# Performance work log

Measured on AMD Instinct MI355X. Metric: run time of the kernel, lower is better.

Reference implementation:

```python
import jax, jax.numpy as jnp
import numpy as np

N, E, IN, H, C, ED = 50000, 400000, 128, 16, 32, 16
NEG_SLOPE = 0.2

def setup_inputs() -> dict:
    key = jax.random.key(0)
    ks = jax.random.split(key, 9)
    x = jax.random.normal(ks[0], (N, IN), jnp.float32)
    edge_index = jax.random.randint(ks[1], (2, E), 0, N, dtype=jnp.int32)
    edge_attr = jax.random.normal(ks[2], (E, ED), jnp.float32)
    batch = jnp.zeros((N,), jnp.int32)
    W_l = jax.random.normal(ks[3], (IN, H * C), jnp.float32) * 0.05
    W_r = jax.random.normal(ks[4], (IN, H * C), jnp.float32) * 0.05
    att = jax.random.normal(ks[5], (H, C), jnp.float32) * 0.05
    bias_gat = jax.random.normal(ks[6], (C,), jnp.float32) * 0.05
    W_res = jax.random.normal(ks[7], (IN, C), jnp.float32) * 0.05
    return {"x": x, "edge_index": edge_index, "edge_attr": edge_attr, "batch": batch,
            "W_l": W_l, "W_r": W_r, "att": att, "bias_gat": bias_gat, "W_res": W_res}

def reference(x, edge_index, edge_attr, batch, W_l, W_r, att, bias_gat, W_res):
    # GATv2Conv (heads=16, concat=False, add_self_loops=True, edge_dim=None so
    # edge_attr is unused; dropout is inference no-op), then ReLU + projected residual.
    n = x.shape[0]
    loops = jnp.arange(n, dtype=edge_index.dtype)
    src = jnp.concatenate([edge_index[0], loops])  # message source j
    dst = jnp.concatenate([edge_index[1], loops])  # message target i
    xl = (x @ W_l).reshape(n, H, C)  # source transform
    xr = (x @ W_r).reshape(n, H, C)  # target transform
    # GATv2 score: e_ij = a^T LeakyReLU(xl_j + xr_i), per head. [Etot, H]
    e = jnp.einsum('ehc,hc->eh', jax.nn.leaky_relu(xl[src] + xr[dst], NEG_SLOPE), att)
    # segment softmax over incoming edges of each destination node
    m = jax.lax.stop_gradient(jax.ops.segment_max(e, dst, num_segments=n))
    ex = jnp.exp(e - m[dst])
    s = jax.ops.segment_sum(ex, dst, num_segments=n)
    alpha = ex / (s[dst] + 1e-16)  # [Etot, H]
    # weighted scatter-aggregate of source messages
    out = jax.ops.segment_sum(xl[src] * alpha[:, :, None], dst, num_segments=n)  # [N, H, C]
    gat_out = out.mean(axis=1) + bias_gat  # concat=False -> head mean, + bias
    x_out = jax.nn.relu(gat_out) + x @ W_res  # ReLU then SkipConnection projection
    return (x_out, alpha)
```

## Files before the change

kernel.cpp:

```cpp
#include <hip/hip_runtime.h>
#include <hip/hip_bf16.h>

typedef unsigned int u32;
typedef unsigned short u16;

typedef __attribute__((ext_vector_type(8))) short bf16x8;
typedef __attribute__((ext_vector_type(4))) float f32x4;
typedef __attribute__((ext_vector_type(2))) float f32x2;

__device__ __forceinline__ float bflo(u32 p){ union{u32 u; float f;} v; v.u = p << 16; return v.f; }
__device__ __forceinline__ float bfhi(u32 p){ union{u32 u; float f;} v; v.u = p & 0xFFFF0000u; return v.f; }
__device__ __forceinline__ u16 f2bf(float f){
    union{float f; u32 u;} v; v.f = f;
    u32 r = (v.u + 0x7FFFu + ((v.u >> 16) & 1u)) >> 16;
    return (u16)r;
}
__device__ __forceinline__ u32 pack2(float a, float b){
    return ((u32)f2bf(a)) | (((u32)f2bf(b)) << 16);
}

#define HH 16
#define CC 32
#define HC 512
#define KIN 128
#define CT 1056
#define RESCALE_THR 8.0f

__global__ __launch_bounds__(256) void k_prep(
    const float* __restrict__ x, const float* __restrict__ Wl,
    const float* __restrict__ Wr, const float* __restrict__ Wres,
    const int* __restrict__ ei,
    u16* __restrict__ xb, u16* __restrict__ wbt_frag, int* __restrict__ counts,
    int xq, int E, int N)
{
    int t = blockIdx.x * 256 + threadIdx.x;
    if (t < xq) {
        const float4* src = (const float4*)(x + (size_t)t * 8);
        float4 a = src[0], b = src[1];
        uint4 o;
        o.x = pack2(a.x, a.y); o.y = pack2(a.z, a.w);
        o.z = pack2(b.x, b.y); o.w = pack2(b.z, b.w);
        ((uint4*)xb)[t] = o;
    } else if (t < xq + CT * 128) {
        int u = t - xq;
        int c = u >> 7;
        int k = u & 127;
        float v;
        if (c < 512)       v = Wl[(size_t)k * 512 + c];
        else if (c < 1024) v = Wr[(size_t)k * 512 + (c - 512)];
        else               v = Wres[(size_t)k * 32 + (c - 1024)];
        int e    = k & 7;
        int krow = k >> 3;
        int kk   = krow >> 2;
        int lane = ((krow & 3) << 4) | (c & 15);
        int ct   = c >> 4;
        wbt_frag[(((size_t)ct * 4 + kk) * 64 + lane) * 8 + e] = f2bf(v);
    } else if (t < xq + CT * 128 + E + N) {
        int e = t - xq - CT * 128;
        int dst = (e < E) ? ei[E + e] : e - E;
        atomicAdd(&counts[dst], 1);
    }
}

__global__ __launch_bounds__(256) void k_mfma(
    const u16* __restrict__ xb, const u16* __restrict__ wbt_frag,
    u16* __restrict__ xl, u16* __restrict__ xr, float* __restrict__ xres,
    int N, int nrb)
{
    __shared__ u16 sh[128 * 128];
    const int i = blockIdx.x;
    const int xcd = i & 7;
    const int j = i >> 3;
    const int rb = xcd + 8 * (j / 9);
    const int cb = j % 9;
    if (rb >= nrb) return;
    const int tid = threadIdx.x;
    const int wave = tid >> 6, lane = tid & 63;
    const int row0 = rb * 128;

    uint4 zero = {0, 0, 0, 0};
    #pragma unroll
    for (int it = 0; it < 8; it++) {
        int idx = tid + it * 256;
        int r = idx >> 4, ch = idx & 15;
        int grow = row0 + r;
        uint4 v = (grow < N) ? ((const uint4*)(xb + (size_t)grow * KIN))[ch] : zero;
        *(uint4*)(sh + r * 128 + ((ch ^ (r & 7)) * 8)) = v;
    }
    __syncthreads();

    bf16x8 afrag[2][4];
    #pragma unroll
    for (int mt = 0; mt < 2; mt++) {
        #pragma unroll
        for (int kk = 0; kk < 4; kk++) {
            int r = wave * 32 + mt * 16 + (lane & 15);
            int chunk = (kk * 4 + (lane >> 4)) ^ (r & 7);
            afrag[mt][kk] = *(const bf16x8*)(sh + r * 128 + chunk * 8);
        }
    }
    __syncthreads();

    if (cb < 8) {
        #pragma unroll
        for (int nt = 0; nt < 8; nt++) {
            int ct = cb * 8 + nt;
            const bf16x8* bp = (const bf16x8*)(wbt_frag + (((size_t)ct * 4) * 64 + lane) * 8);
            f32x4 acc0 = {0, 0, 0, 0}, acc1 = {0, 0, 0, 0};
            #pragma unroll
            for (int kk = 0; kk < 4; kk++) {
                bf16x8 bfrag = bp[kk * 64];
                acc0 = __builtin_amdgcn_mfma_f32_16x16x32_bf16(afrag[0][kk], bfrag, acc0, 0, 0, 0);
                acc1 = __builtin_amdgcn_mfma_f32_16x16x32_bf16(afrag[1][kk], bfrag, acc1, 0, 0, 0);
            }
            int lcol = nt * 16 + (lane & 15);
            int ch = lcol >> 3, cin = lcol & 7;
            #pragma unroll
            for (int mt = 0; mt < 2; mt++) {
                f32x4 a = (mt == 0) ? acc0 : acc1;
                int rbase = wave * 32 + mt * 16 + (lane >> 4) * 4;
                #pragma unroll
                for (int jj = 0; jj < 4; jj++) {
                    int row = rbase + jj;
                    int chs = ch ^ ((row >> 2) & 3);
                    sh[row * 128 + chs * 8 + cin] = f2bf(a[jj]);
                }
            }
        }
        __syncthreads();
        u16* out = (cb < 4) ? xl : xr;
        const int colbase = (cb & 3) * 128;
        #pragma unroll
        for (int it = 0; it < 8; it++) {
            int idx = tid + it * 256;
            int r = idx >> 4, ch = idx & 15;
            int grow = row0 + r;
            if (grow < N) {
                int chs = ch ^ ((r >> 2) & 3);
                uint4 v = *(const uint4*)(sh + r * 128 + chs * 8);
                *(uint4*)(out + (size_t)grow * HC + colbase + ch * 8) = v;
            }
        }
    } else {
        #pragma unroll
        for (int nt = 0; nt < 2; nt++) {
            int ct = 64 + nt;
            const bf16x8* bp = (const bf16x8*)(wbt_frag + (((size_t)ct * 4) * 64 + lane) * 8);
            f32x4 acc0 = {0, 0, 0, 0}, acc1 = {0, 0, 0, 0};
            #pragma unroll
            for (int kk = 0; kk < 4; kk++) {
                bf16x8 bfrag = bp[kk * 64];
                acc0 = __builtin_amdgcn_mfma_f32_16x16x32_bf16(afrag[0][kk], bfrag, acc0, 0, 0, 0);
                acc1 = __builtin_amdgcn_mfma_f32_16x16x32_bf16(afrag[1][kk], bfrag, acc1, 0, 0, 0);
            }
            int c_out = nt * 16 + (lane & 15);
            #pragma unroll
            for (int mt = 0; mt < 2; mt++) {
                f32x4 a = (mt == 0) ? acc0 : acc1;
                int rbse = row0 + wave * 32 + mt * 16 + (lane >> 4) * 4;
                #pragma unroll
                for (int jj = 0; jj < 4; jj++) {
                    int grow = rbse + jj;
                    if (grow < N) xres[(size_t)grow * CC + c_out] = a[jj];
                }
            }
        }
    }
}

__global__ __launch_bounds__(1024) void k_scan1(
    const int* __restrict__ counts, int* __restrict__ offs, int* __restrict__ partials, int N)
{
    __shared__ int sh[1024];
    int i = blockIdx.x * 1024 + threadIdx.x;
    int v = (i < N) ? counts[i] : 0;
    sh[threadIdx.x] = v;
    __syncthreads();
    for (int off = 1; off < 1024; off <<= 1) {
        int t = (threadIdx.x >= off) ? sh[threadIdx.x - off] : 0;
        __syncthreads();
        sh[threadIdx.x] += t;
        __syncthreads();
    }
    if (i < N) offs[i] = sh[threadIdx.x] - v;
    if (threadIdx.x == 1023) partials[blockIdx.x] = sh[1023];
}

__global__ __launch_bounds__(1024) void k_scan3f(
    int* __restrict__ offs, const int* __restrict__ partials,
    int* __restrict__ cursor, int N, int nb)
{
    __shared__ int sbase;
    if (threadIdx.x < 64) {
        int k = threadIdx.x;
        int v = (k < nb && k < blockIdx.x) ? partials[k] : 0;
        #pragma unroll
        for (int st = 1; st < 64; st <<= 1) v += __shfl_xor(v, st);
        if (threadIdx.x == 0) sbase = v;
    }
    __syncthreads();
    int i = blockIdx.x * 1024 + threadIdx.x;
    if (i < N) {
        int o = offs[i] + sbase;
        offs[i] = o;
        cursor[i] = o;
    }
}

__global__ __launch_bounds__(256) void k_scatter(
    const int* __restrict__ ei, int* __restrict__ cursor,
    int* __restrict__ src_sorted, int* __restrict__ eid_sorted, int E, int N)
{
    int e = blockIdx.x * 256 + threadIdx.x;
    if (e >= E + N) return;
    int src, dst;
    if (e < E) { src = ei[e]; dst = ei[E + e]; }
    else       { src = e - E; dst = src; }
    int pos = atomicAdd(&cursor[dst], 1);
    src_sorted[pos] = src;
    eid_sorted[pos] = e;
}

__global__ __launch_bounds__(64) void k_fused(
    const int* __restrict__ src_sorted, const int* __restrict__ eid_sorted,
    const int* __restrict__ offs, const int* __restrict__ counts,
    const u16* __restrict__ xl, const u16* __restrict__ xr, const float* __restrict__ att,
    float* __restrict__ e_out, float2* __restrict__ ms_buf,
    float* __restrict__ out_mean, int N)
{
    const int node = blockIdx.x;
    const int lane = threadIdx.x;
    const int h = lane >> 2;

    uint4 b = ((const uint4*)(xr + (size_t)node * HC))[lane];
    f32x2 xr0 = {bflo(b.x), bfhi(b.x)}, xr1 = {bflo(b.y), bfhi(b.y)};
    f32x2 xr2 = {bflo(b.z), bfhi(b.z)}, xr3 = {bflo(b.w), bfhi(b.w)};
    float4 w0 = ((const float4*)att)[lane * 2];
    float4 w1 = ((const float4*)att)[lane * 2 + 1];
    f32x2 wv0 = {w0.x, w0.y}, wv1 = {w0.z, w0.w};
    f32x2 wv2 = {w1.x, w1.y}, wv3 = {w1.z, w1.w};

    float m = -3.402823466e38f, s = 0.f;
    f32x2 ac0 = {0,0}, ac1 = {0,0}, ac2 = {0,0}, ac3 = {0,0};

    const int beg = offs[node];
    const int deg = counts[node];

    int sv = src_sorted[beg];
    uint4 a = ((const uint4*)(xl + (size_t)sv * HC))[lane];
    for (int t = 0; t < deg; t++) {
        uint4 acr = a;
        int sn = src_sorted[beg + min(t + 1, deg - 1)];
        a = ((const uint4*)(xl + (size_t)sn * HC))[lane];

        f32x2 xv0 = {bflo(acr.x), bfhi(acr.x)};
        f32x2 xv1 = {bflo(acr.y), bfhi(acr.y)};
        f32x2 xv2 = {bflo(acr.z), bfhi(acr.z)};
        f32x2 xv3 = {bflo(acr.w), bfhi(acr.w)};

        f32x2 es2 = {0.f, 0.f};
        f32x2 v;
        v = xv0 + xr0; v = __builtin_elementwise_max(v, 0.2f * v); es2 = __builtin_elementwise_fma(v, wv0, es2);
        v = xv1 + xr1; v = __builtin_elementwise_max(v, 0.2f * v); es2 = __builtin_elementwise_fma(v, wv1, es2);
        v = xv2 + xr2; v = __builtin_elementwise_max(v, 0.2f * v); es2 = __builtin_elementwise_fma(v, wv2, es2);
        v = xv3 + xr3; v = __builtin_elementwise_max(v, 0.2f * v); es2 = __builtin_elementwise_fma(v, wv3, es2);
        float esum = es2.x + es2.y;
        esum += __shfl_xor(esum, 1);
        esum += __shfl_xor(esum, 2);

        int eid = eid_sorted[beg + t];
        if ((lane & 3) == 0)
            e_out[(size_t)eid * HH + h] = esum;

        if (__any(esum > m + RESCALE_THR)) {
            float mn = fmaxf(m, esum);
            float sc = __expf(m - mn);
            float p  = __expf(esum - mn);
            s = s * sc + p;
            m = mn;
            f32x2 p2 = {p, p}, sc2 = {sc, sc};
            ac0 = __builtin_elementwise_fma(p2, xv0, ac0 * sc2);
            ac1 = __builtin_elementwise_fma(p2, xv1, ac1 * sc2);
            ac2 = __builtin_elementwise_fma(p2, xv2, ac2 * sc2);
            ac3 = __builtin_elementwise_fma(p2, xv3, ac3 * sc2);
        } else {
            float p = __expf(esum - m);
            s += p;
            f32x2 p2 = {p, p};
            ac0 = __builtin_elementwise_fma(p2, xv0, ac0);
            ac1 = __builtin_elementwise_fma(p2, xv1, ac1);
            ac2 = __builtin_elementwise_fma(p2, xv2, ac2);
            ac3 = __builtin_elementwise_fma(p2, xv3, ac3);
        }
    }

    float inv = 1.f / (s + 1e-16f);
    if ((lane & 3) == 0)
        ms_buf[(size_t)node * HH + h] = make_float2(m, inv);

    float acc[8] = { ac0.x * inv, ac0.y * inv, ac1.x * inv, ac1.y * inv,
                     ac2.x * inv, ac2.y * inv, ac3.x * inv, ac3.y * inv };
    #pragma unroll
    for (int st = 4; st <= 32; st <<= 1) {
        #pragma unroll
        for (int q = 0; q < 8; q++) acc[q] += __shfl_xor(acc[q], st);
    }
    if (lane < 4) {
        float* dp = out_mean + (size_t)node * CC + lane * 8;
        #pragma unroll
        for (int q = 0; q < 8; q++) dp[q] = acc[q];
    }
}

__global__ __launch_bounds__(256) void k_alphafinal(
    const int* __restrict__ ei, float* __restrict__ alpha,
    const float2* __restrict__ ms_buf, const float* __restrict__ out_mean,
    const float* __restrict__ xres, const float* __restrict__ bias,
    float* __restrict__ x_out, int E, int N)
{
    long long i = (long long)blockIdx.x * 256 + threadIdx.x;
    if (i < (long long)N * CC) {
        int c = (int)(i & 31);
        float g = out_mean[i] * (1.f / 16.f) + bias[c];
        g = g > 0.f ? g : 0.f;
        x_out[i] = g + xres[i];
    }
    long long tot = (long long)(E + N) * HH;
    if (i < tot) {
        int edge = (int)(i >> 4);
        int h = (int)(i & 15);
        int dst = (edge < E) ? ei[E + edge] : edge - E;
        float2 ms = ms_buf[(size_t)dst * HH + h];
        alpha[i] = __expf(alpha[i] - ms.x) * ms.y;
    }
}

extern "C" void kernel_launch(void* const* d_in, const int* in_sizes, int n_in,
                              void* d_out, int out_size, void* d_ws, size_t ws_size,
                              hipStream_t stream)
{
    const int N = in_sizes[0] / KIN;
    const int E = in_sizes[1] / 2;
    const int Etot = E + N;

    const float* x    = (const float*)d_in[0];
    const int*   ei   = (const int*)d_in[1];
    const float* Wl   = (const float*)d_in[4];
    const float* Wr   = (const float*)d_in[5];
    const float* att  = (const float*)d_in[6];
    const float* bias = (const float*)d_in[7];
    const float* Wres = (const float*)d_in[8];

    char* ws = (char*)d_ws;
    u16*   xl         = (u16*)ws;   ws += (size_t)N * HC * 2;
    u16*   xr         = (u16*)ws;   ws += (size_t)N * HC * 2;
    float2* ms_buf    = (float2*)ws; ws += (size_t)N * HH * 8;
    float* xres       = (float*)ws; ws += (size_t)N * CC * 4;
    float* out_mean   = (float*)ws; ws += (size_t)N * CC * 4;
    int*   counts     = (int*)ws;   ws += (size_t)N * 4;
    int*   offs       = (int*)ws;   ws += (size_t)N * 4;
    int*   cursor     = (int*)ws;   ws += (size_t)N * 4;
    int*   partials   = (int*)ws;   ws += 256;
    int*   src_sorted = (int*)ws;   ws += (size_t)Etot * 4;
    int*   eid_sorted = (int*)ws;   ws += (size_t)Etot * 4;
    u16*   xb         = (u16*)ws;   ws += (size_t)N * KIN * 2;
    u16*   wbt_frag   = (u16*)ws;   ws += (size_t)CT * KIN * 2;

    float* x_out     = (float*)d_out;
    float* alpha_out = x_out + (size_t)N * CC;

    hipMemsetAsync(counts, 0, (size_t)N * 4, stream);

    int xq = N * KIN / 8;
    int ptot = xq + CT * 128 + Etot;
    k_prep<<<(ptot + 255) / 256, 256, 0, stream>>>(
        x, Wl, Wr, Wres, ei, xb, wbt_frag, counts, xq, E, N);

    int nrb = (N + 127) / 128;
    int mgrid = 8 * ((nrb + 7) / 8) * 9;
    k_mfma<<<mgrid, 256, 0, stream>>>(xb, wbt_frag, xl, xr, xres, N, nrb);

    int nb = (N + 1023) / 1024;
    k_scan1<<<nb, 1024, 0, stream>>>(counts, offs, partials, N);
    k_scan3f<<<nb, 1024, 0, stream>>>(offs, partials, cursor, N, nb);
    int eg = (Etot + 255) / 256;
    k_scatter<<<eg, 256, 0, stream>>>(ei, cursor, src_sorted, eid_sorted, E, N);

    k_fused<<<N, 64, 0, stream>>>(
        src_sorted, eid_sorted, offs, counts, xl, xr, att,
        alpha_out, ms_buf, out_mean, N);

    long long tot = (long long)Etot * HH;
    k_alphafinal<<<(int)((tot + 255) / 256), 256, 0, stream>>>(
        ei, alpha_out, ms_buf, out_mean, xres, bias, x_out, E, N);
}
```

Before: 193.0 us.

## Process two edges per wavefront iteration by splitting lanes into halves

The fused attention/aggregation kernel now has each half of the 64-lane wavefront handle a different incoming edge, with each lane covering 16 channels instead of 8. This halves the number of serial loop iterations per node and the reduction shuffles per edge. Afterwards the two halves merge their online-softmax state (max, sum, accumulators) with cross-half shuffles. The cost is more registers per lane and wasted work on the masked second half when the degree is odd.

```diff
diff --git a/kernel.cpp b/kernel.cpp
--- a/kernel.cpp
+++ b/kernel.cpp
@@ -230,85 +230,117 @@
 {
     const int node = blockIdx.x;
     const int lane = threadIdx.x;
-    const int h = lane >> 2;
-
-    uint4 b = ((const uint4*)(xr + (size_t)node * HC))[lane];
-    f32x2 xr0 = {bflo(b.x), bfhi(b.x)}, xr1 = {bflo(b.y), bfhi(b.y)};
-    f32x2 xr2 = {bflo(b.z), bfhi(b.z)}, xr3 = {bflo(b.w), bfhi(b.w)};
-    float4 w0 = ((const float4*)att)[lane * 2];
-    float4 w1 = ((const float4*)att)[lane * 2 + 1];
-    f32x2 wv0 = {w0.x, w0.y}, wv1 = {w0.z, w0.w};
-    f32x2 wv2 = {w1.x, w1.y}, wv3 = {w1.z, w1.w};
+    const int l    = lane & 31;
+    const int half = lane >> 5;
+    const int h    = l >> 1;
+
+    const uint4* xr4 = (const uint4*)(xr + (size_t)node * HC) + l * 2;
+    uint4 b0 = xr4[0], b1 = xr4[1];
+    f32x2 xrv[8] = { {bflo(b0.x),bfhi(b0.x)}, {bflo(b0.y),bfhi(b0.y)},
+                     {bflo(b0.z),bfhi(b0.z)}, {bflo(b0.w),bfhi(b0.w)},
+                     {bflo(b1.x),bfhi(b1.x)}, {bflo(b1.y),bfhi(b1.y)},
+                     {bflo(b1.z),bfhi(b1.z)}, {bflo(b1.w),bfhi(b1.w)} };
+    const float4* att4 = (const float4*)att + l * 4;
+    float4 w0 = att4[0], w1 = att4[1], w2 = att4[2], w3 = att4[3];
+    f32x2 wv[8] = { {w0.x,w0.y},{w0.z,w0.w},{w1.x,w1.y},{w1.z,w1.w},
+                    {w2.x,w2.y},{w2.z,w2.w},{w3.x,w3.y},{w3.z,w3.w} };
 
     float m = -3.402823466e38f, s = 0.f;
-    f32x2 ac0 = {0,0}, ac1 = {0,0}, ac2 = {0,0}, ac3 = {0,0};
+    f32x2 ac[8] = { {0,0},{0,0},{0,0},{0,0},{0,0},{0,0},{0,0},{0,0} };
 
     const int beg = offs[node];
     const int deg = counts[node];
 
-    int sv = src_sorted[beg];
-    uint4 a = ((const uint4*)(xl + (size_t)sv * HC))[lane];
-    for (int t = 0; t < deg; t++) {
-        uint4 acr = a;
-        int sn = src_sorted[beg + min(t + 1, deg - 1)];
-        a = ((const uint4*)(xl + (size_t)sn * HC))[lane];
-
-        f32x2 xv0 = {bflo(acr.x), bfhi(acr.x)};
-        f32x2 xv1 = {bflo(acr.y), bfhi(acr.y)};
-        f32x2 xv2 = {bflo(acr.z), bfhi(acr.z)};
-        f32x2 xv3 = {bflo(acr.w), bfhi(acr.w)};
-
-        f32x2 es2 = {0.f, 0.f};
-        f32x2 v;
-        v = xv0 + xr0; v = __builtin_elementwise_max(v, 0.2f * v); es2 = __builtin_elementwise_fma(v, wv0, es2);
-        v = xv1 + xr1; v = __builtin_elementwise_max(v, 0.2f * v); es2 = __builtin_elementwise_fma(v, wv1, es2);
-        v = xv2 + xr2; v = __builtin_elementwise_max(v, 0.2f * v); es2 = __builtin_elementwise_fma(v, wv2, es2);
-        v = xv3 + xr3; v = __builtin_elementwise_max(v, 0.2f * v); es2 = __builtin_elementwise_fma(v, wv3, es2);
-        float esum = es2.x + es2.y;
+    int te = min(half, deg - 1);
+    {
+        int sv = src_sorted[beg + te];
+        const uint4* ap = (const uint4*)(xl + (size_t)sv * HC) + l * 2;
+        b0 = ap[0]; b1 = ap[1];
+    }
+    for (int t0 = 0; t0 < deg; t0 += 2) {
+        uint4 c0 = b0, c1 = b1;
+        bool valid = (t0 + half) < deg;
+        {
+            int sn = src_sorted[beg + min(t0 + 2 + half, deg - 1)];
+            const uint4* np = (const uint4*)(xl + (size_t)sn * HC) + l * 2;
+            b0 = np[0]; b1 = np[1];
+        }
+        f32x2 xv[8] = { {bflo(c0.x),bfhi(c0.x)}, {bflo(c0.y),bfhi(c0.y)},
+                        {bflo(c0.z),bfhi(c0.z)}, {bflo(c0.w),bfhi(c0.w)},
+                        {bflo(c1.x),bfhi(c1.x)}, {bflo(c1.y),bfhi(c1.y)},
+                        {bflo(c1.z),bfhi(c1.z)}, {bflo(c1.w),bfhi(c1.w)} };
+        f32x2 es = {0.f, 0.f};
+        #pragma unroll
+        for (int q = 0; q < 8; q++) {
+            f32x2 v = xv[q] + xrv[q];
+            v = __builtin_elementwise_max(v, 0.2f * v);
+            es = __builtin_elementwise_fma(v, wv[q], es);
+        }
+        float esum = es.x + es.y;
         esum += __shfl_xor(esum, 1);
-        esum += __shfl_xor(esum, 2);
-
-        int eid = eid_sorted[beg + t];
-        if ((lane & 3) == 0)
+
+        int eid = eid_sorted[beg + min(t0 + half, deg - 1)];
+        if ((l & 1) == 0 && valid)
             e_out[(size_t)eid * HH + h] = esum;
 
         if (__any(esum > m + RESCALE_THR)) {
             float mn = fmaxf(m, esum);
             float sc = __expf(m - mn);
             float p  = __expf(esum - mn);
+            if (!valid) p = 0.f;
             s = s * sc + p;
             m = mn;
             f32x2 p2 = {p, p}, sc2 = {sc, sc};
-            ac0 = __builtin_elementwise_fma(p2, xv0, ac0 * sc2);
-            ac1 = __builtin_elementwise_fma(p2, xv1, ac1 * sc2);
-            ac2 = __builtin_elementwise_fma(p2, xv2, ac2 * sc2);
-            ac3 = __builtin_elementwise_fma(p2, xv3, ac3 * sc2);
+            #pragma unroll
+            for (int q = 0; q < 8; q++)
+                ac[q] = __builtin_elementwise_fma(p2, xv[q], ac[q] * sc2);
         } else {
             float p = __expf(esum - m);
+            if (!valid) p = 0.f;
             s += p;
             f32x2 p2 = {p, p};
-            ac0 = __builtin_elementwise_fma(p2, xv0, ac0);
-            ac1 = __builtin_elementwise_fma(p2, xv1, ac1);
-            ac2 = __builtin_elementwise_fma(p2, xv2, ac2);
-            ac3 = __builtin_elementwise_fma(p2, xv3, ac3);
-        }
+            #pragma unroll
+            for (int q = 0; q < 8; q++)
+                ac[q] = __builtin_elementwise_fma(p2, xv[q], ac[q]);
+        }
+    }
+
+    float mo = __shfl_xor(m, 32);
+    float mx = fmaxf(m, mo);
+    float sc = __expf(m - mx);
+    s *= sc;
+    s += __shfl_xor(s, 32);
+    f32x2 sc2 = {sc, sc};
+    #pragma unroll
+    for (int q = 0; q < 8; q++) {
+        f32x2 t = ac[q] * sc2;
+        t.x += __shfl_xor(t.x, 32);
+        t.y += __shfl_xor(t.y, 32);
+        ac[q] = t;
     }
 
     float inv = 1.f / (s + 1e-16f);
-    if ((lane & 3) == 0)
-        ms_buf[(size_t)node * HH + h] = make_float2(m, inv);
-
-    float acc[8] = { ac0.x * inv, ac0.y * inv, ac1.x * inv, ac1.y * inv,
-                     ac2.x * inv, ac2.y * inv, ac3.x * inv, ac3.y * inv };
+    if (lane < 32 && (l & 1) == 0)
+        ms_buf[(size_t)node * HH + h] = make_float2(mx, inv);
+
+    f32x2 inv2 = {inv, inv};
     #pragma unroll
-    for (int st = 4; st <= 32; st <<= 1) {
-        #pragma unroll
-        for (int q = 0; q < 8; q++) acc[q] += __shfl_xor(acc[q], st);
-    }
-    if (lane < 4) {
-        float* dp = out_mean + (size_t)node * CC + lane * 8;
-        #pragma unroll
-        for (int q = 0; q < 8; q++) dp[q] = acc[q];
+    for (int q = 0; q < 8; q++) ac[q] = ac[q] * inv2;
+
+    #pragma unroll
+    for (int st = 2; st <= 16; st <<= 1) {
+        #pragma unroll
+        for (int q = 0; q < 8; q++) {
+            ac[q].x += __shfl_xor(ac[q].x, st);
+            ac[q].y += __shfl_xor(ac[q].y, st);
+        }
+    }
+    if (lane < 2) {
+        float4* dp = (float4*)(out_mean + (size_t)node * CC + lane * 16);
+        dp[0] = make_float4(ac[0].x, ac[0].y, ac[1].x, ac[1].y);
+        dp[1] = make_float4(ac[2].x, ac[2].y, ac[3].x, ac[3].y);
+        dp[2] = make_float4(ac[4].x, ac[4].y, ac[5].x, ac[5].y);
+        dp[3] = make_float4(ac[6].x, ac[6].y, ac[7].x, ac[7].y);
     }
 }
 
```

Result: slower. 210.8 us (+9.2%).
